# Optimization experiments

Hardware: AMD Instinct MI355X
Metric: run time of the kernel (lower is better)

Reference implementation:

```python
import jax, jax.numpy as jnp
import numpy as np

NUM_HEADS = 4
HEAD_DIM = 32


def _conv3x3(x, w, b):
    # x: (N,C,H,W), w: (O,I,3,3) -> SAME padding, stride 1
    y = jax.lax.conv_general_dilated(x, w, window_strides=(1, 1), padding='SAME',
                                     dimension_numbers=('NCHW', 'OIHW', 'NCHW'))
    return y + b[None, :, None, None]


def setup_inputs() -> dict:
    key = jax.random.key(0)
    ks = jax.random.split(key, 15)
    s = 0.05
    return {
        'bev': jax.random.normal(ks[0], (2, 4, 128, 32, 32), jnp.float32),
        'hd_map': jax.random.normal(ks[1], (2, 4, 64, 32, 32), jnp.float32),
        'ego_info': jax.random.normal(ks[2], (2, 4, 16), jnp.float32),
        'front_view_feature': jax.random.normal(ks[3], (2, 4, 64, 16, 16), jnp.float32),
        'w_bev': jax.random.normal(ks[4], (128, 144, 3, 3), jnp.float32) * s,
        'b_bev': jax.random.normal(ks[5], (128,), jnp.float32) * s,
        'w_hd': jax.random.normal(ks[6], (128, 64, 3, 3), jnp.float32) * s,
        'b_hd': jax.random.normal(ks[7], (128,), jnp.float32) * s,
        'wq': jax.random.normal(ks[8], (128, 128), jnp.float32) * s,
        'wk': jax.random.normal(ks[9], (128, 192), jnp.float32) * s,
        'wv': jax.random.normal(ks[10], (128, 192), jnp.float32) * s,
        'wo': jax.random.normal(ks[11], (128, 128), jnp.float32) * s,
        'bo': jax.random.normal(ks[12], (128,), jnp.float32) * s,
        'w_out': jax.random.normal(ks[13], (128, 144, 3, 3), jnp.float32) * s,
        'b_out': jax.random.normal(ks[14], (128,), jnp.float32) * s,
    }


def reference(bev, hd_map, ego_info, front_view_feature,
              w_bev, b_bev, w_hd, b_hd, wq, wk, wv, wo, bo, w_out, b_out):
    B, T, D, H, W = bev.shape
    _, _, C_map, H_map, W_map = hd_map.shape
    _, _, D_front, H_f, W_f = front_view_feature.shape
    E = ego_info.shape[-1]

    # ego broadcast to spatial grid and concat with bev
    ego_sp = jnp.broadcast_to(ego_info[:, :, :, None, None], (B, T, E, H, W))
    bev_with_ego = jnp.concatenate([bev, ego_sp], axis=2).reshape(B * T, D + E, H, W)

    bev_feat = jax.nn.relu(_conv3x3(bev_with_ego, w_bev, b_bev))  # (BT,F,H,W)
    hd_feat = jax.nn.relu(_conv3x3(hd_map.reshape(B * T, C_map, H_map, W_map), w_hd, b_hd))
    F_dim = bev_feat.shape[1]

    # bilinear resize of front view to HD-map grid (align_corners=False semantics)
    front = front_view_feature.reshape(B * T, D_front, H_f, W_f)
    front = jax.image.resize(front, (B * T, D_front, H_map, W_map), method='bilinear')

    kv = jnp.concatenate([hd_feat.reshape(B, T, F_dim, H_map, W_map),
                          front.reshape(B, T, D_front, H_map, W_map)], axis=2)

    # cross attention: query = bev features, key/value = hd-map + front fusion
    q = bev_feat.reshape(B, T, F_dim, H * W).transpose(0, 1, 3, 2)        # (B,T,Nq,F)
    k_in = kv.reshape(B, T, F_dim + D_front, H_map * W_map).transpose(0, 1, 3, 2)  # (B,T,Nk,C)

    Q = jnp.einsum('btnc,oc->btno', q, wq).reshape(B, T, H * W, NUM_HEADS, HEAD_DIM)
    K = jnp.einsum('btnc,oc->btno', k_in, wk).reshape(B, T, H_map * W_map, NUM_HEADS, HEAD_DIM)
    V = jnp.einsum('btnc,oc->btno', k_in, wv).reshape(B, T, H_map * W_map, NUM_HEADS, HEAD_DIM)
    Q = Q.transpose(0, 1, 3, 2, 4)  # (B,T,h,Nq,d)
    K = K.transpose(0, 1, 3, 2, 4)
    V = V.transpose(0, 1, 3, 2, 4)

    scale = HEAD_DIM ** (-0.5)
    scores = jnp.einsum('bthqd,bthkd->bthqk', Q, K) * scale
    probs = jax.nn.softmax(scores, axis=-1)
    attn = jnp.einsum('bthqk,bthkd->bthqd', probs, V)
    attn = attn.transpose(0, 1, 3, 2, 4).reshape(B, T, H * W, NUM_HEADS * HEAD_DIM)
    fused = jnp.einsum('btnc,oc->btno', attn, wo) + bo
    fused = fused.transpose(0, 1, 3, 2).reshape(B, T, F_dim, H, W)

    fused_final = jnp.concatenate([fused, ego_sp], axis=2).reshape(B * T, F_dim + E, H, W)
    out = jax.nn.relu(_conv3x3(fused_final, w_out, b_out))
    return out.reshape(B, T, -1, H, W)
```

## Files before the change

### kernel.cpp

```cpp
#include <hip/hip_runtime.h>
#include <math.h>


#define OFF_QBF 0u
#define OFF_KBF 524288u
#define OFF_VTB 1048576u
#define OFF_FRN 1572864u
#define OFF_XT1 1835008u
#define OFF_XT2 2426880u
#define OFF_XT3 2722816u
#define OFF_WB1 3314688u
#define OFF_WB2 3388416u
#define OFF_WB3 3425280u
#define OFF_WQP 3499008u
#define OFF_WKP 3507200u
#define OFF_WVP 3519488u
#define OFF_WOP 3531776u
#define OFF_E1  3539968u
#define OFF_E2  3549184u
#define OFF_E3  3558400u

typedef short s16x8 __attribute__((ext_vector_type(8)));
typedef float f32x4 __attribute__((ext_vector_type(4)));

__device__ __forceinline__ unsigned short f2bf(float f) {
    unsigned u = __float_as_uint(f);
    unsigned r = (u + 0x7fffu + ((u >> 16) & 1u)) >> 16;
    return (unsigned short)r;
}

__device__ __forceinline__ void gl_lds16(const void* g, void* l) {
    __builtin_amdgcn_global_load_lds(
        (const __attribute__((address_space(1))) unsigned int*)g,
        (__attribute__((address_space(3))) unsigned int*)l, 16, 0, 0);
}

struct MegaParams {
    const float *bev, *hd, *ego, *front;
    const float *w_bev, *b_bev, *w_hd, *b_hd;
    const float *wq, *wk, *wv, *wo, *bo, *w_out, *b_out;
    float* out;
    float* ws;
};

__device__ __forceinline__ void stage0_prep(const MegaParams& p, int start, int stride)
{
    float* ws = p.ws;
    unsigned short* frn = (unsigned short*)(ws + OFF_FRN);
    unsigned short* xT1 = (unsigned short*)(ws + OFF_XT1);
    unsigned short* xT2 = (unsigned short*)(ws + OFF_XT2);
    unsigned short* xT3 = (unsigned short*)(ws + OFF_XT3);
    unsigned short* Wb1 = (unsigned short*)(ws + OFF_WB1);
    unsigned short* Wb2 = (unsigned short*)(ws + OFF_WB2);
    unsigned short* Wb3 = (unsigned short*)(ws + OFF_WB3);
    unsigned short* Wqb = (unsigned short*)(ws + OFF_WQP);
    unsigned short* Wkb = (unsigned short*)(ws + OFF_WKP);
    unsigned short* Wvb = (unsigned short*)(ws + OFF_WVP);
    unsigned short* Wob = (unsigned short*)(ws + OFF_WOP);
    float* E1 = ws + OFF_E1;
    float* E2 = ws + OFF_E2;
    float* E3 = ws + OFF_E3;

    for (int gid = start; gid < 782592; gid += stride) {
        if (gid < 42240) {
            int idx = gid;
            unsigned short* base; int CH, chunk, bt, cell;
            if (idx < 16896)      { base = xT1; CH = 128; bt = idx / 2112; int r2 = idx % 2112; cell = r2 >> 4; chunk = r2 & 15; }
            else if (idx < 25344) { int i2 = idx - 16896; base = xT2; CH = 64; bt = i2 / 1056; int r2 = i2 % 1056; cell = r2 >> 3; chunk = r2 & 7; }
            else                  { int i2 = idx - 25344; base = xT3; CH = 128; bt = i2 / 2112; int r2 = i2 % 2112; cell = r2 >> 4; chunk = r2 & 15; }
            int ty, tx;
            if (cell < 34)      { ty = 0;  tx = cell; }
            else if (cell < 68) { ty = 33; tx = cell - 34; }
            else { int b2 = cell - 68; ty = 1 + (b2 >> 1); tx = (b2 & 1) * 33; }
            s16x8 z = (s16x8)0;
            *(s16x8*)(base + ((size_t)(bt * 34 + ty) * 34 + tx) * CH + chunk * 8) = z;
        } else if (gid < 520448) {
            int g2 = gid - 42240;
            if (g2 < 368640) {
                const float* w; unsigned short* dst; int C, Cin, idx;
                if (g2 < 147456)      { w = p.w_bev; dst = Wb1; C = 128; Cin = 144; idx = g2; }
                else if (g2 < 221184) { w = p.w_hd;  dst = Wb2; C = 64;  Cin = 64;  idx = g2 - 147456; }
                else                  { w = p.w_out; dst = Wb3; C = 128; Cin = 144; idx = g2 - 221184; }
                int tap = idx / (128 * C);
                int rem = idx - tap * 128 * C;
                int oc = rem / C, ic = rem - oc * C;
                dst[idx] = f2bf(w[((size_t)oc * Cin + ic) * 9 + tap]);
            } else if (g2 < 385024) { int i = g2 - 368640; Wqb[i] = f2bf(p.wq[i] * 0.1767766953f); }
            else if (g2 < 409600)   { int i = g2 - 385024; Wkb[i] = f2bf(p.wk[i]); }
            else if (g2 < 434176)   { int i = g2 - 409600; Wvb[i] = f2bf(p.wv[i]); }
            else if (g2 < 450560)   { int i = g2 - 434176; Wob[i] = f2bf(p.wo[i]); }
            else {
                int rem0 = g2 - 450560;
                int which = rem0 / 9216;
                int rem = rem0 - which * 9216;
                int bt = rem / 1152;
                int r2 = rem - bt * 1152;
                int oc = r2 / 9, cls = r2 - oc * 9;
                int rcc = cls / 3, ccc = cls - rcc * 3;
                if (which == 1) { E2[rem] = p.b_hd[oc]; continue; }
                const float* w = (which == 0) ? p.w_bev : p.w_out;
                const float* b = (which == 0) ? p.b_bev : p.b_out;
                float* E = (which == 0) ? E1 : E3;
                int kyLo = (rcc == 0) ? 1 : 0, kyHi = (rcc == 2) ? 1 : 2;
                int kxLo = (ccc == 0) ? 1 : 0, kxHi = (ccc == 2) ? 1 : 2;
                float s = b[oc];
                for (int j = 0; j < 16; ++j) {
                    float ev = p.ego[bt * 16 + j];
                    const float* wp = w + ((size_t)oc * 144 + 128 + j) * 9;
                    float t = 0.f;
                    for (int ky = kyLo; ky <= kyHi; ++ky)
                        for (int kx = kxLo; kx <= kxHi; ++kx)
                            t += wp[ky * 3 + kx];
                    s += ev * t;
                }
                E[rem] = s;
            }
        } else {
            int g3 = gid - 520448;
            if (g3 < 131072) {
                int px_ = g3 & 1023, ch = (g3 >> 10) & 15, bt = g3 >> 14;
                int py = px_ >> 5, pxx = px_ & 31;
                const float* sp = p.bev + (size_t)bt * 131072 + ((size_t)ch << 13) + px_;
                s16x8 v;
                #pragma unroll
                for (int j = 0; j < 8; ++j) v[j] = (short)f2bf(sp[(size_t)j << 10]);
                *(s16x8*)(xT1 + ((size_t)(bt * 34 + py + 1) * 34 + pxx + 1) * 128 + ch * 8) = v;
            } else if (g3 < 196608) {
                int t = g3 - 131072;
                int px_ = t & 1023, ch = (t >> 10) & 7, bt = t >> 13;
                int py = px_ >> 5, pxx = px_ & 31;
                const float* sp = p.hd + (size_t)bt * 65536 + ((size_t)ch << 13) + px_;
                s16x8 v;
                #pragma unroll
                for (int j = 0; j < 8; ++j) v[j] = (short)f2bf(sp[(size_t)j << 10]);
                *(s16x8*)(xT2 + ((size_t)(bt * 34 + py + 1) * 34 + pxx + 1) * 64 + ch * 8) = v;
            } else {
                int t = g3 - 196608;
                int oct = t & 7, pix = (t >> 3) & 1023, bt = t >> 13;
                int oy = pix >> 5, ox = pix & 31;
                float sy = 0.5f * oy - 0.25f, sx = 0.5f * ox - 0.25f;
                int iy0 = (int)floorf(sy); float fy = sy - iy0;
                int ix0 = (int)floorf(sx); float fx = sx - ix0;
                int iy1 = iy0 + 1, ix1 = ix0 + 1;
                iy0 = max(iy0, 0); iy1 = min(iy1, 15);
                ix0 = max(ix0, 0); ix1 = min(ix1, 15);
                float w00 = (1.f - fy) * (1.f - fx), w01 = (1.f - fy) * fx;
                float w10 = fy * (1.f - fx), w11 = fy * fx;
                const float* fp = p.front + ((size_t)(bt * 64 + oct * 8)) * 256;
                s16x8 v;
                #pragma unroll
                for (int j = 0; j < 8; ++j) {
                    const float* f1 = fp + j * 256;
                    float val = w00 * f1[iy0 * 16 + ix0] + w01 * f1[iy0 * 16 + ix1]
                              + w10 * f1[iy1 * 16 + ix0] + w11 * f1[iy1 * 16 + ix1];
                    v[j] = (short)f2bf(val);
                }
                *(s16x8*)(frn + ((size_t)(bt * 1024) + pix) * 64 + oct * 8) = v;
            }
        }
    }
}

template <int C, int ROUNDS, int OUTMODE>
__device__ __forceinline__ void conv4w(
    const unsigned short* __restrict__ xbt, const unsigned short* __restrict__ Wb,
    const float* __restrict__ Ebt, float* __restrict__ outbt,
    char* __restrict__ stag, char* __restrict__ nmajb, int pt, int tid)
{
    const int wave = tid >> 6, lane = tid & 63;
    const int l15 = lane & 15, g = lane >> 4;
    const int ry = wave >> 1, och = wave & 1;

    f32x4 acc[4][2];
    #pragma unroll
    for (int a = 0; a < 4; ++a) { acc[a][0] = (f32x4)0.f; acc[a][1] = (f32x4)0.f; }

    for (int kb = 0; kb < ROUNDS; ++kb) {
        const int ic0 = kb * 32;
        __syncthreads();
        #pragma unroll
        for (int i = 0; i < 3; ++i) {
            int ci = i * 256 + tid;
            if (ci < 544) {
                int e = ci >> 2, s = ci & 3;
                int cch = s ^ ((e + (e >> 2)) & 3);
                int ty = e / 34, tx = e - ty * 34;
                const unsigned short* src =
                    xbt + ((size_t)(pt * 2 + ty) * 34 + tx) * C + ic0 + cch * 8;
                gl_lds16(src, stag + (i * 256 + wave * 64) * 16);
            }
        }
        __syncthreads();

        #pragma unroll
        for (int tap = 0; tap < 9; ++tap) {
            const int ky = tap / 3, kx = tap - ky * 3;
            s16x8 af[4], bf[2];
            #pragma unroll
            for (int fm = 0; fm < 4; ++fm)
                af[fm] = *(const s16x8*)(Wb +
                    ((size_t)(tap * 128 + och * 64 + fm * 16 + l15)) * C + ic0 + g * 8);
            #pragma unroll
            for (int fn = 0; fn < 2; ++fn) {
                int e = (ry + ky) * 34 + fn * 16 + l15 + kx;
                int byte = e * 64 + ((g ^ ((e + (e >> 2)) & 3)) << 4);
                bf[fn] = *(const s16x8*)(stag + byte);
            }
            #pragma unroll
            for (int fm = 0; fm < 4; ++fm)
                #pragma unroll
                for (int fn = 0; fn < 2; ++fn)
                    acc[fm][fn] = __builtin_amdgcn_mfma_f32_16x16x32_bf16(
                        af[fm], bf[fn], acc[fm][fn], 0, 0, 0);
        }
    }

    const int r = pt * 2 + ry;
    const int rc = (r == 0) ? 0 : ((r == 31) ? 2 : 1);
    #pragma unroll
    for (int fn = 0; fn < 2; ++fn) {
        const int c = fn * 16 + l15;
        const int cc = (c == 0) ? 0 : ((c == 31) ? 2 : 1);
        #pragma unroll
        for (int fm = 0; fm < 4; ++fm) {
            if (OUTMODE == 0) {
                #pragma unroll
                for (int rr = 0; rr < 4; ++rr) {
                    int oc = och * 64 + fm * 16 + g * 4 + rr;
                    float v = acc[fm][fn][rr] + Ebt[oc * 9 + rc * 3 + cc];
                    outbt[((size_t)oc << 10) + r * 32 + c] = fmaxf(v, 0.f);
                }
            } else {
                int n_local = ry * 32 + c;
                ushort4 pk;
                #pragma unroll
                for (int rr = 0; rr < 4; ++rr) {
                    int oc = och * 64 + fm * 16 + g * 4 + rr;
                    float v = fmaxf(acc[fm][fn][rr] + Ebt[oc * 9 + rc * 3 + cc], 0.f);
                    ((unsigned short*)&pk)[rr] = f2bf(v);
                }
                int bir = (och * 128 + fm * 32 + g * 8) ^ ((n_local & 7) << 4);
                *(ushort4*)(nmajb + n_local * 256 + bir) = pk;
            }
        }
    }
}

__device__ __forceinline__ void stage1_convproj(const MegaParams& p, char* smem,
                                                int blk, int tid)
{
    if (blk >= 256) return;
    float* ws = p.ws;
    unsigned short* Qbf  = (unsigned short*)(ws + OFF_QBF);
    unsigned short* Kbf  = (unsigned short*)(ws + OFF_KBF);
    unsigned short* VTbf = (unsigned short*)(ws + OFF_VTB);
    unsigned short* frn  = (unsigned short*)(ws + OFF_FRN);
    unsigned short* xT1  = (unsigned short*)(ws + OFF_XT1);
    unsigned short* xT2  = (unsigned short*)(ws + OFF_XT2);
    unsigned short* Wb1  = (unsigned short*)(ws + OFF_WB1);
    unsigned short* Wb2  = (unsigned short*)(ws + OFF_WB2);
    unsigned short* Wqb  = (unsigned short*)(ws + OFF_WQP);
    unsigned short* Wkb  = (unsigned short*)(ws + OFF_WKP);
    unsigned short* Wvb  = (unsigned short*)(ws + OFF_WVP);
    float* E1 = ws + OFF_E1;
    float* E2 = ws + OFF_E2;

    char* stag  = smem;
    char* nmajb = smem + 8704;
    const int wave = tid >> 6, lane = tid & 63;
    const int l15 = lane & 15, g = lane >> 4;

    if (blk < 128) {
        const int bt = blk >> 4, pt = blk & 15;
        conv4w<128, 4, 1>(xT1 + (size_t)bt * 147968, Wb1, E1 + bt * 1152,
                          nullptr, stag, nmajb, pt, tid);
        __syncthreads();
        const int row = wave * 16 + l15;
        const int n = pt * 64 + row;
        f32x4 aq[8];
        #pragma unroll
        for (int ot = 0; ot < 8; ++ot) aq[ot] = (f32x4)0.f;
        #pragma unroll
        for (int ks = 0; ks < 4; ++ks) {
            s16x8 bfr = *(const s16x8*)(nmajb + row * 256 +
                        ((ks * 64 + g * 16) ^ ((row & 7) << 4)));
            #pragma unroll
            for (int ot = 0; ot < 8; ++ot) {
                s16x8 afr = *(const s16x8*)(Wqb + ((size_t)(ot * 16 + l15)) * 128 + ks * 32 + g * 8);
                aq[ot] = __builtin_amdgcn_mfma_f32_16x16x32_bf16(afr, bfr, aq[ot], 0, 0, 0);
            }
        }
        unsigned short* yp = Qbf + ((size_t)(bt * 1024) + n) * 128;
        #pragma unroll
        for (int ot = 0; ot < 8; ++ot) {
            ushort4 pk;
            pk.x = f2bf(aq[ot][0]); pk.y = f2bf(aq[ot][1]);
            pk.z = f2bf(aq[ot][2]); pk.w = f2bf(aq[ot][3]);
            *(ushort4*)(yp + ot * 16 + g * 4) = pk;
        }
    } else {
        const int b2 = blk - 128;
        const int bt = b2 >> 4, pt = b2 & 15;
        conv4w<64, 2, 1>(xT2 + (size_t)bt * 73984, Wb2, E2 + bt * 1152,
                         nullptr, stag, nmajb, pt, tid);
        __syncthreads();
        const int row = wave * 16 + l15;
        const int n = pt * 64 + row;
        const unsigned short* fext = frn + ((size_t)(bt * 1024) + n) * 64 + g * 8;
        f32x4 ak[8], av[8];
        #pragma unroll
        for (int ot = 0; ot < 8; ++ot) { ak[ot] = (f32x4)0.f; av[ot] = (f32x4)0.f; }
        #pragma unroll
        for (int ks = 0; ks < 6; ++ks) {
            s16x8 bfr;
            if (ks < 4)
                bfr = *(const s16x8*)(nmajb + row * 256 +
                      ((ks * 64 + g * 16) ^ ((row & 7) << 4)));
            else
                bfr = *(const s16x8*)(fext + (ks - 4) * 32);
            #pragma unroll
            for (int ot = 0; ot < 8; ++ot) {
                s16x8 afk = *(const s16x8*)(Wkb + ((size_t)(ot * 16 + l15)) * 192 + ks * 32 + g * 8);
                ak[ot] = __builtin_amdgcn_mfma_f32_16x16x32_bf16(afk, bfr, ak[ot], 0, 0, 0);
                s16x8 afv = *(const s16x8*)(Wvb + ((size_t)(ot * 16 + l15)) * 192 + ks * 32 + g * 8);
                av[ot] = __builtin_amdgcn_mfma_f32_16x16x32_bf16(afv, bfr, av[ot], 0, 0, 0);
            }
        }
        unsigned short* kp = Kbf + ((size_t)(bt * 1024) + n) * 128;
        #pragma unroll
        for (int ot = 0; ot < 8; ++ot) {
            ushort4 pk;
            pk.x = f2bf(ak[ot][0]); pk.y = f2bf(ak[ot][1]);
            pk.z = f2bf(ak[ot][2]); pk.w = f2bf(ak[ot][3]);
            *(ushort4*)(kp + ot * 16 + g * 4) = pk;
            int h = ot >> 1, d0 = (ot & 1) * 16 + g * 4;
            unsigned short* vp = VTbf + ((size_t)(bt * 4 + h) * 32 + d0) * 1024 + n;
            #pragma unroll
            for (int r = 0; r < 4; ++r) vp[(size_t)r << 10] = f2bf(av[ot][r]);
        }
    }
}

__device__ __forceinline__ void stage2_attn(const MegaParams& p, char* smem,
                                            int blk, int nblocks, int tid)
{
    float* ws = p.ws;
    unsigned short* Qbf  = (unsigned short*)(ws + OFF_QBF);
    unsigned short* Kbf  = (unsigned short*)(ws + OFF_KBF);
    unsigned short* VTbf = (unsigned short*)(ws + OFF_VTB);
    unsigned short* xT3  = (unsigned short*)(ws + OFF_XT3);
    unsigned short* Wob  = (unsigned short*)(ws + OFF_WOP);

    const int wave = tid >> 6, lane = tid & 63;
    const int l15 = lane & 15, g = lane >> 4;
    unsigned short* pl = (unsigned short*)smem + wave * 640;
    char* nmajA = smem + 5120;

    for (int u = blk; u < 512; u += nblocks) {
        const int bt = u & 7, q0 = (u >> 3) * 16;
        const int h = wave;

        s16x8 qf = *(const s16x8*)(Qbf + ((size_t)(bt * 1024 + q0 + l15)) * 128 + h * 32 + g * 8);

        f32x4 accO0 = (f32x4)0.f, accO1 = (f32x4)0.f;
        float m = -INFINITY, lsum = 0.f;

        const unsigned short* kbase = Kbf + (size_t)(bt * 1024) * 128 + h * 32 + g * 8;
        const unsigned short* vbase = VTbf + ((size_t)(bt * 4 + h)) * 32768 + (size_t)l15 * 1024 + g * 8;

        for (int kc = 0; kc < 1024; kc += 32) {
            s16x8 ak0 = *(const s16x8*)(kbase + (size_t)(kc + l15) * 128);
            s16x8 ak1 = *(const s16x8*)(kbase + (size_t)(kc + 16 + l15) * 128);
            s16x8 av0 = *(const s16x8*)(vbase + kc);
            s16x8 av1 = *(const s16x8*)(vbase + 16384 + kc);

            f32x4 s0 = __builtin_amdgcn_mfma_f32_16x16x32_bf16(ak0, qf, (f32x4)0.f, 0, 0, 0);
            f32x4 s1 = __builtin_amdgcn_mfma_f32_16x16x32_bf16(ak1, qf, (f32x4)0.f, 0, 0, 0);

            float mx = fmaxf(fmaxf(fmaxf(s0[0], s0[1]), fmaxf(s0[2], s0[3])),
                             fmaxf(fmaxf(s1[0], s1[1]), fmaxf(s1[2], s1[3])));
            mx = fmaxf(mx, __shfl_xor(mx, 16));
            mx = fmaxf(mx, __shfl_xor(mx, 32));

            if (!__all(mx - m <= 8.f)) {
                float newm = fmaxf(m, mx);
                float f = __expf(m - newm);
                m = newm;
                lsum *= f;
                accO0 *= f; accO1 *= f;
            }

            float pv[8];
            #pragma unroll
            for (int r = 0; r < 4; ++r) { pv[r] = __expf(s0[r] - m); pv[4 + r] = __expf(s1[r] - m); }
            lsum += ((pv[0] + pv[1]) + (pv[2] + pv[3])) + ((pv[4] + pv[5]) + (pv[6] + pv[7]));

            unsigned pk0 = (unsigned)f2bf(pv[0]) | ((unsigned)f2bf(pv[1]) << 16);
            unsigned pk1 = (unsigned)f2bf(pv[2]) | ((unsigned)f2bf(pv[3]) << 16);
            unsigned pk2 = (unsigned)f2bf(pv[4]) | ((unsigned)f2bf(pv[5]) << 16);
            unsigned pk3 = (unsigned)f2bf(pv[6]) | ((unsigned)f2bf(pv[7]) << 16);
            *(uint2*)(pl + l15 * 40 + 4 * g)      = make_uint2(pk0, pk1);
            *(uint2*)(pl + l15 * 40 + 16 + 4 * g) = make_uint2(pk2, pk3);
            s16x8 pb = *(const s16x8*)(pl + l15 * 40 + 8 * g);

            accO0 = __builtin_amdgcn_mfma_f32_16x16x32_bf16(av0, pb, accO0, 0, 0, 0);
            accO1 = __builtin_amdgcn_mfma_f32_16x16x32_bf16(av1, pb, accO1, 0, 0, 0);
        }

        float lt = lsum + __shfl_xor(lsum, 16);
        lt += __shfl_xor(lt, 32);
        float inv = 1.f / lt;

        {
            char* nb = nmajA + l15 * 256;
            ushort4 o0, o1;
            o0.x = f2bf(accO0[0] * inv); o0.y = f2bf(accO0[1] * inv);
            o0.z = f2bf(accO0[2] * inv); o0.w = f2bf(accO0[3] * inv);
            o1.x = f2bf(accO1[0] * inv); o1.y = f2bf(accO1[1] * inv);
            o1.z = f2bf(accO1[2] * inv); o1.w = f2bf(accO1[3] * inv);
            int sw = (l15 & 7) << 4;
            *(ushort4*)(nb + ((h * 64 + g * 8) ^ sw)) = o0;
            *(ushort4*)(nb + ((h * 64 + 32 + g * 8) ^ sw)) = o1;
        }
        __syncthreads();

        f32x4 po[2];
        po[0] = (f32x4)0.f; po[1] = (f32x4)0.f;
        #pragma unroll
        for (int ks = 0; ks < 4; ++ks) {
            s16x8 bfr = *(const s16x8*)(nmajA + l15 * 256 +
                        ((ks * 64 + g * 16) ^ ((l15 & 7) << 4)));
            #pragma unroll
            for (int j = 0; j < 2; ++j) {
                int ot = wave * 2 + j;
                s16x8 afr = *(const s16x8*)(Wob + ((size_t)(ot * 16 + l15)) * 128 + ks * 32 + g * 8);
                po[j] = __builtin_amdgcn_mfma_f32_16x16x32_bf16(afr, bfr, po[j], 0, 0, 0);
            }
        }
        const int pix = q0 + l15;
        const int py = pix >> 5, px = pix & 31;
        unsigned short* yp = xT3 + ((size_t)(bt * 34 + py + 1) * 34 + px + 1) * 128;
        #pragma unroll
        for (int j = 0; j < 2; ++j) {
            int ot = wave * 2 + j;
            float4 b4 = *(const float4*)(p.bo + ot * 16 + g * 4);
            ushort4 pk;
            pk.x = f2bf(po[j][0] + b4.x); pk.y = f2bf(po[j][1] + b4.y);
            pk.z = f2bf(po[j][2] + b4.z); pk.w = f2bf(po[j][3] + b4.w);
            *(ushort4*)(yp + ot * 16 + g * 4) = pk;
        }
        __syncthreads();
    }
}

__device__ __forceinline__ void stage3_conv(const MegaParams& p, char* smem,
                                            int blk, int tid)
{
    if (blk >= 128) return;
    float* ws = p.ws;
    unsigned short* xT3 = (unsigned short*)(ws + OFF_XT3);
    unsigned short* Wb3 = (unsigned short*)(ws + OFF_WB3);
    float* E3 = ws + OFF_E3;
    const int bt = blk >> 4, pt = blk & 15;
    conv4w<128, 4, 0>(xT3 + (size_t)bt * 147968, Wb3, E3 + bt * 1152,
                      p.out + (size_t)bt * 131072, smem, nullptr, pt, tid);
}

__global__ __launch_bounds__(256, 2) void stage0_kernel(MegaParams p) {
    stage0_prep(p, blockIdx.x * 256 + threadIdx.x, gridDim.x * 256);
}
__global__ __launch_bounds__(256, 2) void stage1_kernel(MegaParams p) {
    __shared__ __align__(16) char smem[25088];
    stage1_convproj(p, smem, blockIdx.x, threadIdx.x);
}
__global__ __launch_bounds__(256, 2) void stage2_kernel(MegaParams p) {
    __shared__ __align__(16) char smem[9216];
    stage2_attn(p, smem, blockIdx.x, gridDim.x, threadIdx.x);
}
__global__ __launch_bounds__(256, 2) void stage3_kernel(MegaParams p) {
    __shared__ __align__(16) char smem[8704];
    stage3_conv(p, smem, blockIdx.x, threadIdx.x);
}

extern "C" void kernel_launch(void* const* d_in, const int* in_sizes, int n_in,
                              void* d_out, int out_size, void* d_ws, size_t ws_size,
                              hipStream_t stream)
{
    MegaParams prm;
    prm.bev   = (const float*)d_in[0];
    prm.hd    = (const float*)d_in[1];
    prm.ego   = (const float*)d_in[2];
    prm.front = (const float*)d_in[3];
    prm.w_bev = (const float*)d_in[4];
    prm.b_bev = (const float*)d_in[5];
    prm.w_hd  = (const float*)d_in[6];
    prm.b_hd  = (const float*)d_in[7];
    prm.wq    = (const float*)d_in[8];
    prm.wk    = (const float*)d_in[9];
    prm.wv    = (const float*)d_in[10];
    prm.wo    = (const float*)d_in[11];
    prm.bo    = (const float*)d_in[12];
    prm.w_out = (const float*)d_in[13];
    prm.b_out = (const float*)d_in[14];
    prm.out   = (float*)d_out;
    prm.ws    = (float*)d_ws;

    stage0_kernel<<<512, 256, 0, stream>>>(prm);
    stage1_kernel<<<256, 256, 0, stream>>>(prm);
    stage2_kernel<<<512, 256, 0, stream>>>(prm);
    stage3_kernel<<<128, 256, 0, stream>>>(prm);
}
```

Measured before the change: 200.0 us.

## Split convs to one row per block and software-pipeline attention K/V loads

The conv tiles go from two rows per block to one row per block, doubling the grid for the conv+projection and output conv stages so more CUs are busy on this small problem. The attention loop now handles 64 keys per iteration and prefetches the next chunk's K/V fragments into registers while computing the current one. The stage0 grid is also doubled. The cost is lower weight reuse per block, more redundant halo loads, and higher register pressure in the attention loop.

Result: faster. 173.6 us (-13.2%).

```diff
diff --git a/kernel.cpp b/kernel.cpp
--- a/kernel.cpp
+++ b/kernel.cpp
@@ -27,6 +27,9 @@
     unsigned u = __float_as_uint(f);
     unsigned r = (u + 0x7fffu + ((u >> 16) & 1u)) >> 16;
     return (unsigned short)r;
+}
+__device__ __forceinline__ unsigned pk2bf(float a, float b) {
+    return (unsigned)f2bf(a) | ((unsigned)f2bf(b) << 16);
 }
 
 __device__ __forceinline__ void gl_lds16(const void* g, void* l) {
@@ -162,31 +165,30 @@
 }
 
 template <int C, int ROUNDS, int OUTMODE>
-__device__ __forceinline__ void conv4w(
+__device__ __forceinline__ void conv1row(
     const unsigned short* __restrict__ xbt, const unsigned short* __restrict__ Wb,
     const float* __restrict__ Ebt, float* __restrict__ outbt,
-    char* __restrict__ stag, char* __restrict__ nmajb, int pt, int tid)
+    char* __restrict__ stag, char* __restrict__ nmajb, int pr, int tid)
 {
     const int wave = tid >> 6, lane = tid & 63;
     const int l15 = lane & 15, g = lane >> 4;
-    const int ry = wave >> 1, och = wave & 1;
-
-    f32x4 acc[4][2];
+
+    f32x4 acc[2][2];
     #pragma unroll
-    for (int a = 0; a < 4; ++a) { acc[a][0] = (f32x4)0.f; acc[a][1] = (f32x4)0.f; }
+    for (int a = 0; a < 2; ++a) { acc[a][0] = (f32x4)0.f; acc[a][1] = (f32x4)0.f; }
 
     for (int kb = 0; kb < ROUNDS; ++kb) {
         const int ic0 = kb * 32;
         __syncthreads();
         #pragma unroll
-        for (int i = 0; i < 3; ++i) {
+        for (int i = 0; i < 2; ++i) {
             int ci = i * 256 + tid;
-            if (ci < 544) {
+            if (ci < 408) {
                 int e = ci >> 2, s = ci & 3;
                 int cch = s ^ ((e + (e >> 2)) & 3);
                 int ty = e / 34, tx = e - ty * 34;
                 const unsigned short* src =
-                    xbt + ((size_t)(pt * 2 + ty) * 34 + tx) * C + ic0 + cch * 8;
+                    xbt + ((size_t)(pr + ty) * 34 + tx) * C + ic0 + cch * 8;
                 gl_lds16(src, stag + (i * 256 + wave * 64) * 16);
             }
         }
@@ -195,52 +197,51 @@
         #pragma unroll
         for (int tap = 0; tap < 9; ++tap) {
             const int ky = tap / 3, kx = tap - ky * 3;
-            s16x8 af[4], bf[2];
-            #pragma unroll
-            for (int fm = 0; fm < 4; ++fm)
+            s16x8 af[2], bf[2];
+            #pragma unroll
+            for (int fm = 0; fm < 2; ++fm)
                 af[fm] = *(const s16x8*)(Wb +
-                    ((size_t)(tap * 128 + och * 64 + fm * 16 + l15)) * C + ic0 + g * 8);
-            #pragma unroll
-            for (int fn = 0; fn < 2; ++fn) {
-                int e = (ry + ky) * 34 + fn * 16 + l15 + kx;
+                    ((size_t)(tap * 128 + wave * 32 + fm * 16 + l15)) * C + ic0 + g * 8);
+            #pragma unroll
+            for (int nf = 0; nf < 2; ++nf) {
+                int e = ky * 34 + nf * 16 + l15 + kx;
                 int byte = e * 64 + ((g ^ ((e + (e >> 2)) & 3)) << 4);
-                bf[fn] = *(const s16x8*)(stag + byte);
-            }
-            #pragma unroll
-            for (int fm = 0; fm < 4; ++fm)
-                #pragma unroll
-                for (int fn = 0; fn < 2; ++fn)
-                    acc[fm][fn] = __builtin_amdgcn_mfma_f32_16x16x32_bf16(
-                        af[fm], bf[fn], acc[fm][fn], 0, 0, 0);
+                bf[nf] = *(const s16x8*)(stag + byte);
+            }
+            #pragma unroll
+            for (int fm = 0; fm < 2; ++fm)
+                #pragma unroll
+                for (int nf = 0; nf < 2; ++nf)
+                    acc[fm][nf] = __builtin_amdgcn_mfma_f32_16x16x32_bf16(
+                        af[fm], bf[nf], acc[fm][nf], 0, 0, 0);
         }
     }
 
-    const int r = pt * 2 + ry;
+    const int r = pr;
     const int rc = (r == 0) ? 0 : ((r == 31) ? 2 : 1);
     #pragma unroll
-    for (int fn = 0; fn < 2; ++fn) {
-        const int c = fn * 16 + l15;
+    for (int nf = 0; nf < 2; ++nf) {
+        const int c = nf * 16 + l15;
         const int cc = (c == 0) ? 0 : ((c == 31) ? 2 : 1);
         #pragma unroll
-        for (int fm = 0; fm < 4; ++fm) {
+        for (int fm = 0; fm < 2; ++fm) {
             if (OUTMODE == 0) {
                 #pragma unroll
                 for (int rr = 0; rr < 4; ++rr) {
-                    int oc = och * 64 + fm * 16 + g * 4 + rr;
-                    float v = acc[fm][fn][rr] + Ebt[oc * 9 + rc * 3 + cc];
+                    int oc = wave * 32 + fm * 16 + g * 4 + rr;
+                    float v = acc[fm][nf][rr] + Ebt[oc * 9 + rc * 3 + cc];
                     outbt[((size_t)oc << 10) + r * 32 + c] = fmaxf(v, 0.f);
                 }
             } else {
-                int n_local = ry * 32 + c;
                 ushort4 pk;
                 #pragma unroll
                 for (int rr = 0; rr < 4; ++rr) {
-                    int oc = och * 64 + fm * 16 + g * 4 + rr;
-                    float v = fmaxf(acc[fm][fn][rr] + Ebt[oc * 9 + rc * 3 + cc], 0.f);
+                    int oc = wave * 32 + fm * 16 + g * 4 + rr;
+                    float v = fmaxf(acc[fm][nf][rr] + Ebt[oc * 9 + rc * 3 + cc], 0.f);
                     ((unsigned short*)&pk)[rr] = f2bf(v);
                 }
-                int bir = (och * 128 + fm * 32 + g * 8) ^ ((n_local & 7) << 4);
-                *(ushort4*)(nmajb + n_local * 256 + bir) = pk;
+                int bir = (wave * 64 + fm * 32 + g * 8) ^ ((c & 7) << 4);
+                *(ushort4*)(nmajb + c * 256 + bir) = pk;
             }
         }
     }
@@ -249,7 +250,7 @@
 __device__ __forceinline__ void stage1_convproj(const MegaParams& p, char* smem,
                                                 int blk, int tid)
 {
-    if (blk >= 256) return;
+    if (blk >= 512) return;
     float* ws = p.ws;
     unsigned short* Qbf  = (unsigned short*)(ws + OFF_QBF);
     unsigned short* Kbf  = (unsigned short*)(ws + OFF_KBF);
@@ -266,77 +267,98 @@
     float* E2 = ws + OFF_E2;
 
     char* stag  = smem;
-    char* nmajb = smem + 8704;
+    char* nmajb = smem + 6528;
     const int wave = tid >> 6, lane = tid & 63;
     const int l15 = lane & 15, g = lane >> 4;
 
-    if (blk < 128) {
-        const int bt = blk >> 4, pt = blk & 15;
-        conv4w<128, 4, 1>(xT1 + (size_t)bt * 147968, Wb1, E1 + bt * 1152,
-                          nullptr, stag, nmajb, pt, tid);
+    if (blk < 256) {
+        const int bt = blk >> 5, pr = blk & 31;
+        conv1row<128, 4, 1>(xT1 + (size_t)bt * 147968, Wb1, E1 + bt * 1152,
+                            nullptr, stag, nmajb, pr, tid);
         __syncthreads();
-        const int row = wave * 16 + l15;
-        const int n = pt * 64 + row;
-        f32x4 aq[8];
-        #pragma unroll
-        for (int ot = 0; ot < 8; ++ot) aq[ot] = (f32x4)0.f;
+        f32x4 aq[2][2];
+        aq[0][0] = (f32x4)0.f; aq[0][1] = (f32x4)0.f;
+        aq[1][0] = (f32x4)0.f; aq[1][1] = (f32x4)0.f;
         #pragma unroll
         for (int ks = 0; ks < 4; ++ks) {
-            s16x8 bfr = *(const s16x8*)(nmajb + row * 256 +
-                        ((ks * 64 + g * 16) ^ ((row & 7) << 4)));
-            #pragma unroll
-            for (int ot = 0; ot < 8; ++ot) {
+            s16x8 bfr[2];
+            #pragma unroll
+            for (int nf = 0; nf < 2; ++nf) {
+                int row = nf * 16 + l15;
+                bfr[nf] = *(const s16x8*)(nmajb + row * 256 +
+                          ((ks * 64 + g * 16) ^ ((row & 7) << 4)));
+            }
+            #pragma unroll
+            for (int j = 0; j < 2; ++j) {
+                int ot = wave * 2 + j;
                 s16x8 afr = *(const s16x8*)(Wqb + ((size_t)(ot * 16 + l15)) * 128 + ks * 32 + g * 8);
-                aq[ot] = __builtin_amdgcn_mfma_f32_16x16x32_bf16(afr, bfr, aq[ot], 0, 0, 0);
-            }
-        }
-        unsigned short* yp = Qbf + ((size_t)(bt * 1024) + n) * 128;
-        #pragma unroll
-        for (int ot = 0; ot < 8; ++ot) {
-            ushort4 pk;
-            pk.x = f2bf(aq[ot][0]); pk.y = f2bf(aq[ot][1]);
-            pk.z = f2bf(aq[ot][2]); pk.w = f2bf(aq[ot][3]);
-            *(ushort4*)(yp + ot * 16 + g * 4) = pk;
+                aq[j][0] = __builtin_amdgcn_mfma_f32_16x16x32_bf16(afr, bfr[0], aq[j][0], 0, 0, 0);
+                aq[j][1] = __builtin_amdgcn_mfma_f32_16x16x32_bf16(afr, bfr[1], aq[j][1], 0, 0, 0);
+            }
+        }
+        #pragma unroll
+        for (int nf = 0; nf < 2; ++nf) {
+            unsigned short* yp = Qbf + ((size_t)(bt * 1024 + pr * 32 + nf * 16 + l15)) * 128;
+            #pragma unroll
+            for (int j = 0; j < 2; ++j) {
+                int ot = wave * 2 + j;
+                ushort4 pk;
+                pk.x = f2bf(aq[j][nf][0]); pk.y = f2bf(aq[j][nf][1]);
+                pk.z = f2bf(aq[j][nf][2]); pk.w = f2bf(aq[j][nf][3]);
+                *(ushort4*)(yp + ot * 16 + g * 4) = pk;
+            }
         }
     } else {
-        const int b2 = blk - 128;
-        const int bt = b2 >> 4, pt = b2 & 15;
-        conv4w<64, 2, 1>(xT2 + (size_t)bt * 73984, Wb2, E2 + bt * 1152,
-                         nullptr, stag, nmajb, pt, tid);
+        const int b2 = blk - 256;
+        const int bt = b2 >> 5, pr = b2 & 31;
+        conv1row<64, 2, 1>(xT2 + (size_t)bt * 73984, Wb2, E2 + bt * 1152,
+                           nullptr, stag, nmajb, pr, tid);
         __syncthreads();
-        const int row = wave * 16 + l15;
-        const int n = pt * 64 + row;
-        const unsigned short* fext = frn + ((size_t)(bt * 1024) + n) * 64 + g * 8;
-        f32x4 ak[8], av[8];
-        #pragma unroll
-        for (int ot = 0; ot < 8; ++ot) { ak[ot] = (f32x4)0.f; av[ot] = (f32x4)0.f; }
+        f32x4 ak[2][2], av[2][2];
+        ak[0][0] = (f32x4)0.f; ak[0][1] = (f32x4)0.f;
+        ak[1][0] = (f32x4)0.f; ak[1][1] = (f32x4)0.f;
+        av[0][0] = (f32x4)0.f; av[0][1] = (f32x4)0.f;
+        av[1][0] = (f32x4)0.f; av[1][1] = (f32x4)0.f;
         #pragma unroll
         for (int ks = 0; ks < 6; ++ks) {
-            s16x8 bfr;
-            if (ks < 4)
-                bfr = *(const s16x8*)(nmajb + row * 256 +
-                      ((ks * 64 + g * 16) ^ ((row & 7) << 4)));
-            else
-                bfr = *(const s16x8*)(fext + (ks - 4) * 32);
-            #pragma unroll
-            for (int ot = 0; ot < 8; ++ot) {
+            s16x8 bfr[2];
+            #pragma unroll
+            for (int nf = 0; nf < 2; ++nf) {
+                int row = nf * 16 + l15;
+                if (ks < 4)
+                    bfr[nf] = *(const s16x8*)(nmajb + row * 256 +
+                              ((ks * 64 + g * 16) ^ ((row & 7) << 4)));
+                else
+                    bfr[nf] = *(const s16x8*)(frn +
+                              ((size_t)(bt * 1024 + pr * 32 + row)) * 64 + (ks - 4) * 32 + g * 8);
+            }
+            #pragma unroll
+            for (int j = 0; j < 2; ++j) {
+                int ot = wave * 2 + j;
                 s16x8 afk = *(const s16x8*)(Wkb + ((size_t)(ot * 16 + l15)) * 192 + ks * 32 + g * 8);
-                ak[ot] = __builtin_amdgcn_mfma_f32_16x16x32_bf16(afk, bfr, ak[ot], 0, 0, 0);
                 s16x8 afv = *(const s16x8*)(Wvb + ((size_t)(ot * 16 + l15)) * 192 + ks * 32 + g * 8);
-                av[ot] = __builtin_amdgcn_mfma_f32_16x16x32_bf16(afv, bfr, av[ot], 0, 0, 0);
-            }
-        }
-        unsigned short* kp = Kbf + ((size_t)(bt * 1024) + n) * 128;
-        #pragma unroll
-        for (int ot = 0; ot < 8; ++ot) {
-            ushort4 pk;
-            pk.x = f2bf(ak[ot][0]); pk.y = f2bf(ak[ot][1]);
-            pk.z = f2bf(ak[ot][2]); pk.w = f2bf(ak[ot][3]);
-            *(ushort4*)(kp + ot * 16 + g * 4) = pk;
-            int h = ot >> 1, d0 = (ot & 1) * 16 + g * 4;
-            unsigned short* vp = VTbf + ((size_t)(bt * 4 + h) * 32 + d0) * 1024 + n;
-            #pragma unroll
-            for (int r = 0; r < 4; ++r) vp[(size_t)r << 10] = f2bf(av[ot][r]);
+                ak[j][0] = __builtin_amdgcn_mfma_f32_16x16x32_bf16(afk, bfr[0], ak[j][0], 0, 0, 0);
+                ak[j][1] = __builtin_amdgcn_mfma_f32_16x16x32_bf16(afk, bfr[1], ak[j][1], 0, 0, 0);
+                av[j][0] = __builtin_amdgcn_mfma_f32_16x16x32_bf16(afv, bfr[0], av[j][0], 0, 0, 0);
+                av[j][1] = __builtin_amdgcn_mfma_f32_16x16x32_bf16(afv, bfr[1], av[j][1], 0, 0, 0);
+            }
+        }
+        #pragma unroll
+        for (int nf = 0; nf < 2; ++nf) {
+            const int n = pr * 32 + nf * 16 + l15;
+            unsigned short* kp = Kbf + ((size_t)(bt * 1024) + n) * 128;
+            #pragma unroll
+            for (int j = 0; j < 2; ++j) {
+                int ot = wave * 2 + j;
+                ushort4 pk;
+                pk.x = f2bf(ak[j][nf][0]); pk.y = f2bf(ak[j][nf][1]);
+                pk.z = f2bf(ak[j][nf][2]); pk.w = f2bf(ak[j][nf][3]);
+                *(ushort4*)(kp + ot * 16 + g * 4) = pk;
+                int h = ot >> 1, d0 = (ot & 1) * 16 + g * 4;
+                unsigned short* vp = VTbf + ((size_t)(bt * 4 + h) * 32 + d0) * 1024 + n;
+                #pragma unroll
+                for (int r = 0; r < 4; ++r) vp[(size_t)r << 10] = f2bf(av[j][nf][r]);
+            }
         }
     }
 }
@@ -353,8 +375,8 @@
 
     const int wave = tid >> 6, lane = tid & 63;
     const int l15 = lane & 15, g = lane >> 4;
-    unsigned short* pl = (unsigned short*)smem + wave * 640;
-    char* nmajA = smem + 5120;
+    unsigned short* pl = (unsigned short*)(smem + wave * 2304);
+    char* nmajA = smem + 9216;
 
     for (int u = blk; u < 512; u += nblocks) {
         const int bt = u & 7, q0 = (u >> 3) * 16;
@@ -365,20 +387,43 @@
         f32x4 accO0 = (f32x4)0.f, accO1 = (f32x4)0.f;
         float m = -INFINITY, lsum = 0.f;
 
-        const unsigned short* kbase = Kbf + (size_t)(bt * 1024) * 128 + h * 32 + g * 8;
-        const unsigned short* vbase = VTbf + ((size_t)(bt * 4 + h)) * 32768 + (size_t)l15 * 1024 + g * 8;
-
-        for (int kc = 0; kc < 1024; kc += 32) {
-            s16x8 ak0 = *(const s16x8*)(kbase + (size_t)(kc + l15) * 128);
-            s16x8 ak1 = *(const s16x8*)(kbase + (size_t)(kc + 16 + l15) * 128);
-            s16x8 av0 = *(const s16x8*)(vbase + kc);
-            s16x8 av1 = *(const s16x8*)(vbase + 16384 + kc);
-
-            f32x4 s0 = __builtin_amdgcn_mfma_f32_16x16x32_bf16(ak0, qf, (f32x4)0.f, 0, 0, 0);
-            f32x4 s1 = __builtin_amdgcn_mfma_f32_16x16x32_bf16(ak1, qf, (f32x4)0.f, 0, 0, 0);
-
-            float mx = fmaxf(fmaxf(fmaxf(s0[0], s0[1]), fmaxf(s0[2], s0[3])),
-                             fmaxf(fmaxf(s1[0], s1[1]), fmaxf(s1[2], s1[3])));
+        const unsigned short* kb = Kbf + (size_t)(bt * 1024) * 128 + h * 32 + g * 8;
+        const unsigned short* vb = VTbf + ((size_t)(bt * 4 + h)) * 32768 + (size_t)l15 * 1024 + g * 8;
+
+        s16x8 kf0 = *(const s16x8*)(kb + (size_t)(l15) * 128);
+        s16x8 kf1 = *(const s16x8*)(kb + (size_t)(16 + l15) * 128);
+        s16x8 kf2 = *(const s16x8*)(kb + (size_t)(32 + l15) * 128);
+        s16x8 kf3 = *(const s16x8*)(kb + (size_t)(48 + l15) * 128);
+        s16x8 vf0 = *(const s16x8*)(vb + 0);
+        s16x8 vf1 = *(const s16x8*)(vb + 32);
+        s16x8 vf2 = *(const s16x8*)(vb + 16384);
+        s16x8 vf3 = *(const s16x8*)(vb + 16384 + 32);
+
+        for (int kc = 0; kc < 1024; kc += 64) {
+            s16x8 nk0, nk1, nk2, nk3, nv0, nv1, nv2, nv3;
+            const bool more = (kc < 960);
+            if (more) {
+                int kn = kc + 64;
+                nk0 = *(const s16x8*)(kb + (size_t)(kn + l15) * 128);
+                nk1 = *(const s16x8*)(kb + (size_t)(kn + 16 + l15) * 128);
+                nk2 = *(const s16x8*)(kb + (size_t)(kn + 32 + l15) * 128);
+                nk3 = *(const s16x8*)(kb + (size_t)(kn + 48 + l15) * 128);
+                nv0 = *(const s16x8*)(vb + kn);
+                nv1 = *(const s16x8*)(vb + kn + 32);
+                nv2 = *(const s16x8*)(vb + 16384 + kn);
+                nv3 = *(const s16x8*)(vb + 16384 + kn + 32);
+            }
+
+            f32x4 s0 = __builtin_amdgcn_mfma_f32_16x16x32_bf16(kf0, qf, (f32x4)0.f, 0, 0, 0);
+            f32x4 s1 = __builtin_amdgcn_mfma_f32_16x16x32_bf16(kf1, qf, (f32x4)0.f, 0, 0, 0);
+            f32x4 s2 = __builtin_amdgcn_mfma_f32_16x16x32_bf16(kf2, qf, (f32x4)0.f, 0, 0, 0);
+            f32x4 s3 = __builtin_amdgcn_mfma_f32_16x16x32_bf16(kf3, qf, (f32x4)0.f, 0, 0, 0);
+
+            float mx = fmaxf(
+                fmaxf(fmaxf(fmaxf(s0[0], s0[1]), fmaxf(s0[2], s0[3])),
+                      fmaxf(fmaxf(s1[0], s1[1]), fmaxf(s1[2], s1[3]))),
+                fmaxf(fmaxf(fmaxf(s2[0], s2[1]), fmaxf(s2[2], s2[3])),
+                      fmaxf(fmaxf(s3[0], s3[1]), fmaxf(s3[2], s3[3]))));
             mx = fmaxf(mx, __shfl_xor(mx, 16));
             mx = fmaxf(mx, __shfl_xor(mx, 32));
 
@@ -390,21 +435,43 @@
                 accO0 *= f; accO1 *= f;
             }
 
-            float pv[8];
-            #pragma unroll
-            for (int r = 0; r < 4; ++r) { pv[r] = __expf(s0[r] - m); pv[4 + r] = __expf(s1[r] - m); }
-            lsum += ((pv[0] + pv[1]) + (pv[2] + pv[3])) + ((pv[4] + pv[5]) + (pv[6] + pv[7]));
-
-            unsigned pk0 = (unsigned)f2bf(pv[0]) | ((unsigned)f2bf(pv[1]) << 16);
-            unsigned pk1 = (unsigned)f2bf(pv[2]) | ((unsigned)f2bf(pv[3]) << 16);
-            unsigned pk2 = (unsigned)f2bf(pv[4]) | ((unsigned)f2bf(pv[5]) << 16);
-            unsigned pk3 = (unsigned)f2bf(pv[6]) | ((unsigned)f2bf(pv[7]) << 16);
-            *(uint2*)(pl + l15 * 40 + 4 * g)      = make_uint2(pk0, pk1);
-            *(uint2*)(pl + l15 * 40 + 16 + 4 * g) = make_uint2(pk2, pk3);
-            s16x8 pb = *(const s16x8*)(pl + l15 * 40 + 8 * g);
-
-            accO0 = __builtin_amdgcn_mfma_f32_16x16x32_bf16(av0, pb, accO0, 0, 0, 0);
-            accO1 = __builtin_amdgcn_mfma_f32_16x16x32_bf16(av1, pb, accO1, 0, 0, 0);
+            {
+                float p0 = __expf(s0[0] - m), p1 = __expf(s0[1] - m),
+                      p2 = __expf(s0[2] - m), p3 = __expf(s0[3] - m);
+                lsum += (p0 + p1) + (p2 + p3);
+                *(uint2*)(pl + l15 * 72 + 4 * g) = make_uint2(pk2bf(p0, p1), pk2bf(p2, p3));
+            }
+            {
+                float p0 = __expf(s1[0] - m), p1 = __expf(s1[1] - m),
+                      p2 = __expf(s1[2] - m), p3 = __expf(s1[3] - m);
+                lsum += (p0 + p1) + (p2 + p3);
+                *(uint2*)(pl + l15 * 72 + 16 + 4 * g) = make_uint2(pk2bf(p0, p1), pk2bf(p2, p3));
+            }
+            {
+                float p0 = __expf(s2[0] - m), p1 = __expf(s2[1] - m),
+                      p2 = __expf(s2[2] - m), p3 = __expf(s2[3] - m);
+                lsum += (p0 + p1) + (p2 + p3);
+                *(uint2*)(pl + l15 * 72 + 32 + 4 * g) = make_uint2(pk2bf(p0, p1), pk2bf(p2, p3));
+            }
+            {
+                float p0 = __expf(s3[0] - m), p1 = __expf(s3[1] - m),
+                      p2 = __expf(s3[2] - m), p3 = __expf(s3[3] - m);
+                lsum += (p0 + p1) + (p2 + p3);
+                *(uint2*)(pl + l15 * 72 + 48 + 4 * g) = make_uint2(pk2bf(p0, p1), pk2bf(p2, p3));
+            }
+
+            s16x8 pb0 = *(const s16x8*)(pl + l15 * 72 + g * 8);
+            s16x8 pb1 = *(const s16x8*)(pl + l15 * 72 + 32 + g * 8);
+
+            accO0 = __builtin_amdgcn_mfma_f32_16x16x32_bf16(vf0, pb0, accO0, 0, 0, 0);
+            accO0 = __builtin_amdgcn_mfma_f32_16x16x32_bf16(vf1, pb1, accO0, 0, 0, 0);
+            accO1 = __builtin_amdgcn_mfma_f32_16x16x32_bf16(vf2, pb0, accO1, 0, 0, 0);
+            accO1 = __builtin_amdgcn_mfma_f32_16x16x32_bf16(vf3, pb1, accO1, 0, 0, 0);
+
+            if (more) {
+                kf0 = nk0; kf1 = nk1; kf2 = nk2; kf3 = nk3;
+                vf0 = nv0; vf1 = nv1; vf2 = nv2; vf3 = nv3;
+            }
         }
 
         float lt = lsum + __shfl_xor(lsum, 16);
@@ -456,29 +523,29 @@
 __device__ __forceinline__ void stage3_conv(const MegaParams& p, char* smem,
                                             int blk, int tid)
 {
-    if (blk >= 128) return;
+    if (blk >= 256) return;
     float* ws = p.ws;
     unsigned short* xT3 = (unsigned short*)(ws + OFF_XT3);
     unsigned short* Wb3 = (unsigned short*)(ws + OFF_WB3);
     float* E3 = ws + OFF_E3;
-    const int bt = blk >> 4, pt = blk & 15;
-    conv4w<128, 4, 0>(xT3 + (size_t)bt * 147968, Wb3, E3 + bt * 1152,
-                      p.out + (size_t)bt * 131072, smem, nullptr, pt, tid);
+    const int bt = blk >> 5, pr = blk & 31;
+    conv1row<128, 4, 0>(xT3 + (size_t)bt * 147968, Wb3, E3 + bt * 1152,
+                        p.out + (size_t)bt * 131072, smem, nullptr, pr, tid);
 }
 
 __global__ __launch_bounds__(256, 2) void stage0_kernel(MegaParams p) {
     stage0_prep(p, blockIdx.x * 256 + threadIdx.x, gridDim.x * 256);
 }
 __global__ __launch_bounds__(256, 2) void stage1_kernel(MegaParams p) {
-    __shared__ __align__(16) char smem[25088];
+    __shared__ __align__(16) char smem[14720];
     stage1_convproj(p, smem, blockIdx.x, threadIdx.x);
 }
 __global__ __launch_bounds__(256, 2) void stage2_kernel(MegaParams p) {
-    __shared__ __align__(16) char smem[9216];
+    __shared__ __align__(16) char smem[13312];
     stage2_attn(p, smem, blockIdx.x, gridDim.x, threadIdx.x);
 }
 __global__ __launch_bounds__(256, 2) void stage3_kernel(MegaParams p) {
-    __shared__ __align__(16) char smem[8704];
+    __shared__ __align__(16) char smem[6528];
     stage3_conv(p, smem, blockIdx.x, threadIdx.x);
 }
 
@@ -505,8 +572,8 @@
     prm.out   = (float*)d_out;
     prm.ws    = (float*)d_ws;
 
-    stage0_kernel<<<512, 256, 0, stream>>>(prm);
-    stage1_kernel<<<256, 256, 0, stream>>>(prm);
+    stage0_kernel<<<1024, 256, 0, stream>>>(prm);
+    stage1_kernel<<<512, 256, 0, stream>>>(prm);
     stage2_kernel<<<512, 256, 0, stream>>>(prm);
-    stage3_kernel<<<128, 256, 0, stream>>>(prm);
-}
+    stage3_kernel<<<256, 256, 0, stream>>>(prm);
+}
```
